# Kernel tuning notes

Hardware: AMD Instinct MI355X
Metric: run time of the kernel (lower is better)

## Reference

```python
import jax, jax.numpy as jnp
import numpy as np

ANCHOR = 12.0      # anchor (d,h,w) size used for parametrization
NMS_IOU = 0.25     # suppression threshold
TOPK = 2048        # pre-NMS candidate cap (= stop_after), fixed for jit


def setup_inputs() -> dict:
    key = jax.random.key(0)
    k1, k2 = jax.random.split(key)
    bboxes = jax.random.normal(k1, (2, 6, 64, 96, 96), dtype=jnp.float32)
    scores = jax.random.normal(k2, (2, 64, 96, 96), dtype=jnp.float32)
    return {"bboxes": bboxes, "scores": scores}


def _deparametrize(bboxes):
    # bboxes: (B, 6, D, H, W), parametrized as in Ren et al. 2017
    D, H, W = bboxes.shape[2:]
    axes = [jnp.arange(s, dtype=bboxes.dtype) + 0.5 for s in (D, H, W)]
    zyx = jnp.stack(jnp.meshgrid(*axes, indexing='ij'))        # (3, D, H, W)
    abs_zyx = bboxes[:, :3] * ANCHOR + zyx[None]               # center coords
    abs_dhw = jnp.exp(bboxes[:, 3:]) * ANCHOR                  # sizes
    return jnp.concatenate([abs_zyx, abs_dhw], axis=1)


def _pairwise_iou(b1, b2):
    # b1: (N,6), b2: (M,6) with (z,y,x,d,h,w)
    c1, s1 = b1[:, :3], b1[:, 3:]
    c2, s2 = b2[:, :3], b2[:, 3:]
    lo = jnp.maximum((c1 - s1 / 2)[:, None, :], (c2 - s2 / 2)[None, :, :])
    hi = jnp.minimum((c1 + s1 / 2)[:, None, :], (c2 + s2 / 2)[None, :, :])
    inter = jnp.clip(hi - lo, 0).prod(-1)                      # (N, M)
    union = s1.prod(-1)[:, None] + s2.prod(-1)[None, :] - inter
    return inter / union


def _nms_one(boxes_flat, scores_flat):
    # boxes_flat: (P, 6), scores_flat: (P,)
    scores_top, idx = jax.lax.top_k(scores_flat, TOPK)
    boxes_top = boxes_flat[idx]                                # (K, 6)
    ious = _pairwise_iou(boxes_top, boxes_top)                 # (K, K)
    ar = jnp.arange(TOPK)

    def body(keep, i):
        # suppress lower-scored boxes overlapping a kept box i
        suppress = (ious[i] > NMS_IOU) & (ar > i) & keep[i]
        return keep & ~suppress, None

    keep, _ = jax.lax.scan(body, jnp.ones(TOPK, dtype=bool), ar)
    out = jnp.concatenate([scores_top[:, None], boxes_top], axis=1)  # (K, 7)
    return jnp.where(keep[:, None], out, 0.0)


def reference(bboxes, scores):
    abs_boxes = _deparametrize(bboxes)                         # (B, 6, D, H, W)
    B = bboxes.shape[0]
    boxes_flat = abs_boxes.reshape(B, 6, -1).transpose(0, 2, 1)  # (B, P, 6)
    scores_flat = scores.reshape(B, -1)                          # (B, P)
    # (B, TOPK, 7): column 0 = score, columns 1:7 = (z,y,x,d,h,w); suppressed rows zeroed
    return jax.vmap(_nms_one)(boxes_flat, scores_flat)
```

## Files before the change

kernel.cpp:

```cpp
#include <hip/hip_runtime.h>
#include <math.h>

typedef unsigned int U32;
typedef unsigned long long U64;

constexpr int N_SP   = 64 * 96 * 96;
constexpr int NBATCH = 2;
constexpr int K_TOP  = 2048;
constexpr int NBINS  = 8192;
constexpr int CAP    = 8192;
constexpr float ANCHOR_F = 12.0f;
constexpr float NMS_IOU_F = 0.25f;

constexpr size_t OFF_HIST = 0;
constexpr size_t OFF_CNT  = OFF_HIST + 2 * NBINS * 4;
constexpr size_t OFF_THR  = OFF_CNT + 256;
constexpr size_t OFF_RANK = OFF_THR + 256;
constexpr size_t OFF_CAND = OFF_RANK + 2 * CAP * 4;
constexpr size_t OFF_BOX  = OFF_CAND + 2 * CAP * 8;
constexpr size_t OFF_MASK = OFF_BOX + 2 * 14 * K_TOP * 4;

__device__ __forceinline__ U32 mono_of(float f) {
  U32 u = __float_as_uint(f);
  return (u & 0x80000000u) ? ~u : (u | 0x80000000u);
}
__device__ __forceinline__ float un_mono(U32 m) {
  U32 u = (m & 0x80000000u) ? (m ^ 0x80000000u) : ~m;
  return __uint_as_float(u);
}

__global__ void __launch_bounds__(256) k_zero(U32* hist, U32* rank, U32* cnt) {
  int g = blockIdx.x * 256 + threadIdx.x;
  hist[g] = 0;
  rank[g] = 0;
  if (g < NBATCH) cnt[g] = 0;
}

__global__ void __launch_bounds__(256) k_hist(const float* __restrict__ scores,
                                              U32* __restrict__ hist) {
  int b = blockIdx.y;
  const float4* s4 = (const float4*)(scores + (size_t)b * N_SP)
                     + (size_t)blockIdx.x * 2048 + threadIdx.x;
  float4 v[8];
#pragma unroll
  for (int e = 0; e < 8; ++e) v[e] = s4[e * 256];
  __shared__ U32 lh[NBINS];
  for (int k = threadIdx.x; k < NBINS; k += 256) lh[k] = 0;
  __syncthreads();
#pragma unroll
  for (int e = 0; e < 8; ++e) {
    atomicAdd(&lh[mono_of(v[e].x) >> 19], 1u);
    atomicAdd(&lh[mono_of(v[e].y) >> 19], 1u);
    atomicAdd(&lh[mono_of(v[e].z) >> 19], 1u);
    atomicAdd(&lh[mono_of(v[e].w) >> 19], 1u);
  }
  __syncthreads();
  U32* gh = hist + (size_t)b * NBINS;
  for (int k = threadIdx.x; k < NBINS; k += 256) {
    U32 c = lh[k];
    if (c) atomicAdd(&gh[k], c);
  }
}

__global__ void __launch_bounds__(256) k_thresh(const U32* __restrict__ hist,
                                                U32* __restrict__ thr) {
  int b = blockIdx.x;
  const U32* h = hist + (size_t)b * NBINS;
  __shared__ U32 part[256];
  int t = threadIdx.x;
  int base = NBINS - 32 * (t + 1);
  U32 s = 0;
  for (int k = 0; k < 32; ++k) s += h[base + k];
  part[t] = s;
  __syncthreads();
  if (t == 0) {
    U32 cum = 0, bin = 0;
    for (int c = 0; c < 256; ++c) {
      U32 p = part[c];
      if (cum + p >= (U32)K_TOP) {
        int hb = NBINS - 32 * c - 1;
        for (int k = 0; k < 32; ++k) {
          cum += h[hb - k];
          if (cum >= (U32)K_TOP) { bin = (U32)(hb - k); break; }
        }
        break;
      }
      cum += p;
    }
    thr[b] = bin;
  }
}

__global__ void __launch_bounds__(256) k_collect(const float* __restrict__ scores,
                                                 const U32* __restrict__ thr,
                                                 U32* __restrict__ cnt,
                                                 U64* __restrict__ cand) {
  int b = blockIdx.y;
  U32 tb = thr[b];
  const float4* s4 = (const float4*)(scores + (size_t)b * N_SP)
                     + (size_t)blockIdx.x * 1024 + threadIdx.x;
  float4 v[4];
#pragma unroll
  for (int e = 0; e < 4; ++e) v[e] = s4[e * 256];
  __shared__ U64 lbuf[4096];
  __shared__ U32 lcnt, lbase;
  if (threadIdx.x == 0) lcnt = 0;
  __syncthreads();
#pragma unroll
  for (int e = 0; e < 4; ++e) {
    U32 i0 = (blockIdx.x * 1024 + e * 256 + threadIdx.x) * 4;
    float vv[4] = {v[e].x, v[e].y, v[e].z, v[e].w};
#pragma unroll
    for (int c = 0; c < 4; ++c) {
      U32 m = mono_of(vv[c]);
      if ((m >> 19) >= tb) {
        U32 p = atomicAdd(&lcnt, 1u);
        lbuf[p] = ((U64)m << 32) | (U32)(~(i0 + c));
      }
    }
  }
  __syncthreads();
  if (threadIdx.x == 0 && lcnt) lbase = atomicAdd(&cnt[b], lcnt);
  __syncthreads();
  U32 n = lcnt;
  if (n == 0) return;
  U32 base = lbase;
  U64* cb = cand + (size_t)b * CAP;
  for (U32 k = threadIdx.x; k < n; k += 256) {
    U32 pos = base + k;
    if (pos < (U32)CAP) cb[pos] = lbuf[k];
  }
}

__global__ void __launch_bounds__(256) k_count(const U64* __restrict__ cand,
                                               const U32* __restrict__ cnt,
                                               U32* __restrict__ rank) {
  int b = blockIdx.y;
  U32 C = cnt[b]; if (C > (U32)CAP) C = CAP;
  U32 g = blockIdx.x * 256 + threadIdx.x;
  U32 t = g & (CAP - 1);
  U32 sgm = g >> 13;
  if (t >= C) return;
  const U64* cb = cand + (size_t)b * CAP;
  U64 key = cb[t];
  U32 segLen = (C + 7) >> 3;
  U32 j0 = sgm * segLen;
  U32 j1 = j0 + segLen; if (j1 > C) j1 = C;
  U32 c = 0;
  for (U32 j = j0; j < j1; ++j) c += (cb[j] > key) ? 1u : 0u;
  if (c) atomicAdd(&rank[(size_t)b * CAP + t], c);
}

#pragma clang fp contract(off)

__global__ void __launch_bounds__(256) k_gather(const float* __restrict__ bboxes,
                                                const U64* __restrict__ cand,
                                                const U32* __restrict__ cnt,
                                                const U32* __restrict__ rank,
                                                float* __restrict__ box) {
  int b = blockIdx.y;
  U32 C = cnt[b]; if (C > (U32)CAP) C = CAP;
  U32 t = blockIdx.x * 256 + threadIdx.x;
  if (t >= C) return;
  U32 r = rank[(size_t)b * CAP + t];
  if (r >= (U32)K_TOP) return;
  U64 key = cand[(size_t)b * CAP + t];
  U32 idx = ~(U32)(key & 0xFFFFFFFFull);
  float sc = un_mono((U32)(key >> 32));
  int d = idx / 9216;
  int rem = idx - d * 9216;
  int h = rem / 96;
  int w = rem - h * 96;
  const float* src = bboxes + (size_t)b * 6 * N_SP + idx;
  float r0 = src[0];
  float r1 = src[(size_t)N_SP];
  float r2 = src[(size_t)2 * N_SP];
  float r3 = src[(size_t)3 * N_SP];
  float r4 = src[(size_t)4 * N_SP];
  float r5 = src[(size_t)5 * N_SP];
  float cz = r0 * ANCHOR_F + ((float)d + 0.5f);
  float cy = r1 * ANCHOR_F + ((float)h + 0.5f);
  float cx = r2 * ANCHOR_F + ((float)w + 0.5f);
  float sz = (float)exp((double)r3) * ANCHOR_F;
  float sy = (float)exp((double)r4) * ANCHOR_F;
  float sx = (float)exp((double)r5) * ANCHOR_F;
  float* B0 = box + (size_t)b * 14 * K_TOP;
  B0[0 * K_TOP + r] = cz;  B0[1 * K_TOP + r] = cy;  B0[2 * K_TOP + r] = cx;
  B0[3 * K_TOP + r] = sz;  B0[4 * K_TOP + r] = sy;  B0[5 * K_TOP + r] = sx;
  B0[6 * K_TOP + r] = cz - sz * 0.5f;
  B0[7 * K_TOP + r] = cy - sy * 0.5f;
  B0[8 * K_TOP + r] = cx - sx * 0.5f;
  B0[9 * K_TOP + r] = cz + sz * 0.5f;
  B0[10 * K_TOP + r] = cy + sy * 0.5f;
  B0[11 * K_TOP + r] = cx + sx * 0.5f;
  B0[12 * K_TOP + r] = (sz * sy) * sx;
  B0[13 * K_TOP + r] = sc;
}

__global__ void __launch_bounds__(256) k_mask(const float* __restrict__ box,
                                              U32* __restrict__ mask) {
  int b = blockIdx.y;
  int it = blockIdx.x >> 2;
  int jq = blockIdx.x & 3;
  const float* B0 = box + (size_t)b * 14 * K_TOP;
  __shared__ float ls[7][512];
  int j0 = jq * 512;
  for (int k = threadIdx.x; k < 7 * 512; k += 256) {
    int a = k >> 9, j = k & 511;
    ls[a][j] = B0[(size_t)(6 + a) * K_TOP + j0 + j];
  }
  __syncthreads();
  int lane = threadIdx.x & 63;
  int wv = threadIdx.x >> 6;
  int i = it * 64 + lane;
  float imin0 = B0[6 * K_TOP + i], imin1 = B0[7 * K_TOP + i], imin2 = B0[8 * K_TOP + i];
  float imax0 = B0[9 * K_TOP + i], imax1 = B0[10 * K_TOP + i], imax2 = B0[11 * K_TOP + i];
  float ivol  = B0[12 * K_TOP + i];
  U32 wbits[4];
  int jb = wv * 128;
#pragma unroll
  for (int wl = 0; wl < 4; ++wl) {
    U32 bits = 0;
    for (int bit = 0; bit < 32; ++bit) {
      int jl = jb + wl * 32 + bit;
      int j = j0 + jl;
      float lo0 = fmaxf(imin0, ls[0][jl]);
      float lo1 = fmaxf(imin1, ls[1][jl]);
      float lo2 = fmaxf(imin2, ls[2][jl]);
      float hi0 = fminf(imax0, ls[3][jl]);
      float hi1 = fminf(imax1, ls[4][jl]);
      float hi2 = fminf(imax2, ls[5][jl]);
      float d0 = fmaxf(hi0 - lo0, 0.0f);
      float d1 = fmaxf(hi1 - lo1, 0.0f);
      float d2 = fmaxf(hi2 - lo2, 0.0f);
      float inter = (d0 * d1) * d2;
      float uni = (ivol + ls[6][jl]) - inter;
      float iou = inter / uni;
      bits |= ((iou > NMS_IOU_F) && (j > i)) ? (1u << bit) : 0u;
    }
    wbits[wl] = bits;
  }
  uint4* mrow = (uint4*)(mask + ((size_t)(b * K_TOP + i)) * 64);
  mrow[jq * 4 + wv] = make_uint4(wbits[0], wbits[1], wbits[2], wbits[3]);
}

__global__ void __launch_bounds__(256) k_nms(const float* __restrict__ box,
                                             const U32* __restrict__ mask,
                                             float* __restrict__ out) {
  int b = blockIdx.x;
  int tid = threadIdx.x;
  const U32* mk = mask + (size_t)b * K_TOP * 64;
  __shared__ U32 buf[2][128 * 64];
  {
    const uint4* g = (const uint4*)mk;
    uint4* dst = (uint4*)buf[0];
    for (int k = tid; k < 2048; k += 256) dst[k] = g[k];
  }
  __syncthreads();
  U32 keep = 0xFFFFFFFFu;
  for (int c = 0; c < 16; ++c) {
    if (tid >= 64) {
      if (c + 1 < 16) {
        const uint4* g = (const uint4*)(mk + (size_t)(c + 1) * 8192);
        uint4* dst = (uint4*)buf[(c + 1) & 1];
        for (int k = tid - 64; k < 2048; k += 192) dst[k] = g[k];
      }
    } else {
      const U32* bs = buf[c & 1];
      for (int wb = 0; wb < 4; ++wb) {
        int w = c * 4 + wb;
        U32 kw = __shfl(keep, w);
#pragma unroll
        for (int bit = 0; bit < 32; ++bit) {
          U32 m = bs[(wb * 32 + bit) * 64 + tid];
          U32 mw = __shfl(m, w);
          U32 neg = (kw & (1u << bit)) ? 0xFFFFFFFFu : 0u;
          keep &= ~(m & neg);
          kw &= ~(mw & neg);
        }
      }
    }
    __syncthreads();
  }
  U32* keepArr = &buf[0][0];
  if (tid < 64) keepArr[tid] = keep;
  __syncthreads();
  const float* B0 = box + (size_t)b * 14 * K_TOP;
  for (int t = tid; t < K_TOP; t += 256) {
    U32 kp = (keepArr[t >> 5] >> (t & 31)) & 1u;
    float sc = B0[13 * K_TOP + t];
    float vz = B0[0 * K_TOP + t], vy = B0[1 * K_TOP + t], vx = B0[2 * K_TOP + t];
    float dz = B0[3 * K_TOP + t], dy = B0[4 * K_TOP + t], dx = B0[5 * K_TOP + t];
    float* o = out + (size_t)(b * K_TOP + t) * 7;
    o[0] = kp ? sc : 0.0f;
    o[1] = kp ? vz : 0.0f;
    o[2] = kp ? vy : 0.0f;
    o[3] = kp ? vx : 0.0f;
    o[4] = kp ? dz : 0.0f;
    o[5] = kp ? dy : 0.0f;
    o[6] = kp ? dx : 0.0f;
  }
}

extern "C" void kernel_launch(void* const* d_in, const int* in_sizes, int n_in,
                              void* d_out, int out_size, void* d_ws, size_t ws_size,
                              hipStream_t stream) {
  const float* bboxes = (const float*)d_in[0];
  const float* scores = (const float*)d_in[1];
  float* out = (float*)d_out;

  char* ws = (char*)d_ws;
  U32* hist = (U32*)(ws + OFF_HIST);
  U32* cnt  = (U32*)(ws + OFF_CNT);
  U32* thr  = (U32*)(ws + OFF_THR);
  U32* rank = (U32*)(ws + OFF_RANK);
  U64* cand = (U64*)(ws + OFF_CAND);
  float* box = (float*)(ws + OFF_BOX);
  U32* mask = (U32*)(ws + OFF_MASK);

  k_zero<<<64, 256, 0, stream>>>(hist, rank, cnt);
  k_hist<<<dim3(72, NBATCH), 256, 0, stream>>>(scores, hist);
  k_thresh<<<NBATCH, 256, 0, stream>>>(hist, thr);
  k_collect<<<dim3(144, NBATCH), 256, 0, stream>>>(scores, thr, cnt, cand);
  k_count<<<dim3(256, NBATCH), 256, 0, stream>>>(cand, cnt, rank);
  k_gather<<<dim3(CAP / 256, NBATCH), 256, 0, stream>>>(bboxes, cand, cnt, rank, box);
  k_mask<<<dim3(128, NBATCH), 256, 0, stream>>>(box, mask);
  k_nms<<<NBATCH, 256, 0, stream>>>(box, mask, out);
}
```

Before: 201.8 us.

## Transpose suppression mask and resolve NMS words with scalar readlane

The IoU mask is now written transposed (word-major, box-minor). The NMS kernel stages it into XOR-swizzled shared memory so each lane reads the 32 rows of its own word. Each 32-box word group is resolved on the diagonal word with scalar readlane operations, then applied to all lanes with one OR-reduction. This replaces the serial per-bit shuffle chain, shortening the dependent critical path at the cost of more registers and scattered global mask writes.

```diff
diff --git a/kernel.cpp b/kernel.cpp
--- a/kernel.cpp
+++ b/kernel.cpp
@@ -240,8 +240,12 @@
     }
     wbits[wl] = bits;
   }
-  uint4* mrow = (uint4*)(mask + ((size_t)(b * K_TOP + i)) * 64);
-  mrow[jq * 4 + wv] = make_uint4(wbits[0], wbits[1], wbits[2], wbits[3]);
+  U32* mT = mask + (size_t)b * 64 * K_TOP;
+#pragma unroll
+  for (int wl = 0; wl < 4; ++wl) {
+    int w = jq * 16 + wv * 4 + wl;
+    mT[(size_t)w * K_TOP + i] = wbits[wl];
+  }
 }
 
 __global__ void __launch_bounds__(256) k_nms(const float* __restrict__ box,
@@ -249,35 +253,66 @@
                                              float* __restrict__ out) {
   int b = blockIdx.x;
   int tid = threadIdx.x;
-  const U32* mk = mask + (size_t)b * K_TOP * 64;
-  __shared__ U32 buf[2][128 * 64];
-  {
-    const uint4* g = (const uint4*)mk;
-    uint4* dst = (uint4*)buf[0];
-    for (int k = tid; k < 2048; k += 256) dst[k] = g[k];
-  }
-  __syncthreads();
+  const U32* mkT = mask + (size_t)b * 64 * K_TOP;
+  __shared__ U32 buf[2][64 * 128];
+
+  for (int k = tid; k < 2048; k += 256) {
+    int w = k >> 5, seg = k & 31;
+    uint4 v = *(const uint4*)(mkT + (size_t)w * K_TOP + seg * 4);
+    U32* d = &buf[0][w * 128];
+    int r0 = seg * 4, sw = w & 31;
+    d[(r0 + 0) ^ sw] = v.x;
+    d[(r0 + 1) ^ sw] = v.y;
+    d[(r0 + 2) ^ sw] = v.z;
+    d[(r0 + 3) ^ sw] = v.w;
+  }
+  __syncthreads();
+
   U32 keep = 0xFFFFFFFFu;
   for (int c = 0; c < 16; ++c) {
     if (tid >= 64) {
       if (c + 1 < 16) {
-        const uint4* g = (const uint4*)(mk + (size_t)(c + 1) * 8192);
-        uint4* dst = (uint4*)buf[(c + 1) & 1];
-        for (int k = tid - 64; k < 2048; k += 192) dst[k] = g[k];
+        U32* dstbuf = buf[(c + 1) & 1];
+        for (int k = tid - 64; k < 2048; k += 192) {
+          int w = k >> 5, seg = k & 31;
+          uint4 v = *(const uint4*)(mkT + (size_t)w * K_TOP + (c + 1) * 128 + seg * 4);
+          U32* d = &dstbuf[w * 128];
+          int r0 = seg * 4, sw = w & 31;
+          d[(r0 + 0) ^ sw] = v.x;
+          d[(r0 + 1) ^ sw] = v.y;
+          d[(r0 + 2) ^ sw] = v.z;
+          d[(r0 + 3) ^ sw] = v.w;
+        }
       }
     } else {
-      const U32* bs = buf[c & 1];
-      for (int wb = 0; wb < 4; ++wb) {
-        int w = c * 4 + wb;
-        U32 kw = __shfl(keep, w);
-#pragma unroll
-        for (int bit = 0; bit < 32; ++bit) {
-          U32 m = bs[(wb * 32 + bit) * 64 + tid];
-          U32 mw = __shfl(m, w);
-          U32 neg = (kw & (1u << bit)) ? 0xFFFFFFFFu : 0u;
-          keep &= ~(m & neg);
-          kw &= ~(mw & neg);
+      const U32* row = &buf[c & 1][tid * 128];
+      U32 swz = (U32)(tid & 31);
+      U32 rw[32];
+#pragma unroll
+      for (int q = 0; q < 32; ++q) rw[q] = row[(U32)q ^ swz];
+#pragma unroll
+      for (int kk = 0; kk < 4; ++kk) {
+        U32 nx[32];
+        if (kk < 3) {
+#pragma unroll
+          for (int q = 0; q < 32; ++q) nx[q] = row[(U32)((kk + 1) * 32 + q) ^ swz];
         }
+        int g = c * 4 + kk;
+        U32 kw = (U32)__builtin_amdgcn_readlane((int)keep, g);
+        U32 dg[32];
+#pragma unroll
+        for (int q = 0; q < 32; ++q) dg[q] = (U32)__builtin_amdgcn_readlane((int)rw[q], g);
+#pragma unroll
+        for (int q = 0; q < 32; ++q) kw = (kw & (1u << q)) ? (kw & ~dg[q]) : kw;
+        U32 acc = 0;
+#pragma unroll
+        for (int q = 0; q < 32; ++q) {
+          U32 sel = (kw & (1u << q)) ? 0xFFFFFFFFu : 0u;
+          acc |= sel & rw[q];
+        }
+        keep &= ~acc;
+#pragma unroll
+        for (int q = 0; q < 32; ++q) if (kk < 3) rw[q] = nx[q];
       }
     }
     __syncthreads();
```

After: 214.6 us. 1.06x slower.

## Rewrite NMS sweep as single-wave register pipeline with readlane block resolution

Applied to the files above, without the earlier changes.

The greedy suppression sweep now runs in a single 64-lane wave. Mask rows are streamed directly from global memory into four rotating register buffers, replacing the LDS double buffer, the producer waves and the per-chunk block barriers. Within each 32-box diagonal block, the diagonal words are broadcast with readlane and resolved in a scalar-style serial loop, followed by one OR-reduction to apply suppression. This removes per-bit shuffles and the syncthreads calls, but it raises register pressure (128+ VGPRs) and relies on enough loads in flight to hide global latency.

```diff
diff --git a/kernel.cpp b/kernel.cpp
--- a/kernel.cpp
+++ b/kernel.cpp
@@ -250,41 +250,53 @@
   int b = blockIdx.x;
   int tid = threadIdx.x;
   const U32* mk = mask + (size_t)b * K_TOP * 64;
-  __shared__ U32 buf[2][128 * 64];
-  {
-    const uint4* g = (const uint4*)mk;
-    uint4* dst = (uint4*)buf[0];
-    for (int k = tid; k < 2048; k += 256) dst[k] = g[k];
-  }
-  __syncthreads();
-  U32 keep = 0xFFFFFFFFu;
-  for (int c = 0; c < 16; ++c) {
-    if (tid >= 64) {
-      if (c + 1 < 16) {
-        const uint4* g = (const uint4*)(mk + (size_t)(c + 1) * 8192);
-        uint4* dst = (uint4*)buf[(c + 1) & 1];
-        for (int k = tid - 64; k < 2048; k += 192) dst[k] = g[k];
-      }
-    } else {
-      const U32* bs = buf[c & 1];
-      for (int wb = 0; wb < 4; ++wb) {
-        int w = c * 4 + wb;
-        U32 kw = __shfl(keep, w);
-#pragma unroll
-        for (int bit = 0; bit < 32; ++bit) {
-          U32 m = bs[(wb * 32 + bit) * 64 + tid];
-          U32 mw = __shfl(m, w);
-          U32 neg = (kw & (1u << bit)) ? 0xFFFFFFFFu : 0u;
-          keep &= ~(m & neg);
-          kw &= ~(mw & neg);
-        }
-      }
+  __shared__ U32 keepArr[64];
+
+  if (tid < 64) {
+    int lane = tid;
+    U32 keep = 0xFFFFFFFFu;
+    U32 bufA[32], bufB[32], bufC[32], bufD[32];
+
+#define LOADB(R, blk)                                                          \
+  do {                                                                         \
+    if ((blk) < 64) {                                                          \
+      _Pragma("unroll") for (int q = 0; q < 32; ++q)                           \
+          R[q] = mk[((size_t)((blk) * 32 + q)) * 64 + lane];                   \
+    }                                                                          \
+  } while (0)
+
+#define COMPUTE(R, g)                                                          \
+  do {                                                                         \
+    U32 kw = (U32)__builtin_amdgcn_readlane((int)keep, (g));                   \
+    U32 dg[32];                                                                \
+    _Pragma("unroll") for (int q = 0; q < 32; ++q)                             \
+        dg[q] = (U32)__builtin_amdgcn_readlane((int)R[q], (g));                \
+    _Pragma("unroll") for (int q = 0; q < 32; ++q)                             \
+        kw = (kw & (1u << q)) ? (kw & ~dg[q]) : kw;                            \
+    U32 acc = 0;                                                               \
+    _Pragma("unroll") for (int q = 0; q < 32; ++q) {                           \
+      U32 sel = (kw & (1u << q)) ? 0xFFFFFFFFu : 0u;                           \
+      acc |= sel & R[q];                                                       \
+    }                                                                          \
+    keep &= ~acc;                                                              \
+  } while (0)
+
+    LOADB(bufA, 0);
+    LOADB(bufB, 1);
+    LOADB(bufC, 2);
+    LOADB(bufD, 3);
+    for (int g = 0; g < 64; g += 4) {
+      COMPUTE(bufA, g);     LOADB(bufA, g + 4);
+      COMPUTE(bufB, g + 1); LOADB(bufB, g + 5);
+      COMPUTE(bufC, g + 2); LOADB(bufC, g + 6);
+      COMPUTE(bufD, g + 3); LOADB(bufD, g + 7);
     }
-    __syncthreads();
-  }
-  U32* keepArr = &buf[0][0];
-  if (tid < 64) keepArr[tid] = keep;
-  __syncthreads();
+#undef LOADB
+#undef COMPUTE
+    keepArr[lane] = keep;
+  }
+  __syncthreads();
+
   const float* B0 = box + (size_t)b * 14 * K_TOP;
   for (int t = tid; t < K_TOP; t += 256) {
     U32 kp = (keepArr[t >> 5] >> (t & 31)) & 1u;
```

Measured after the change: 202.0 us. Within noise of the previous version (+0.1%).

## Use scalar readlane diagonal resolve and direct global-to-LDS loads in NMS scan

Applied to the files above, without the earlier changes.

The serial NMS scan used to do a per-bit shuffle chain for each 32-bit word. It now loads 32 mask rows into registers and resolves the diagonal word with scalar readlanes on a uniform keep word. It then ORs the kept rows into one accumulator, which cuts the serial dependency chain and removes the cross-lane shuffles. The mask staging also switches to the global_load_lds builtin, which writes 16-byte loads from global memory straight into LDS without going through VGPRs. The cost is higher register pressure from the two 32-element arrays.

```diff
diff --git a/kernel.cpp b/kernel.cpp
--- a/kernel.cpp
+++ b/kernel.cpp
@@ -249,42 +249,61 @@
                                              float* __restrict__ out) {
   int b = blockIdx.x;
   int tid = threadIdx.x;
+  int wv = tid >> 6, lane = tid & 63;
   const U32* mk = mask + (size_t)b * K_TOP * 64;
-  __shared__ U32 buf[2][128 * 64];
-  {
-    const uint4* g = (const uint4*)mk;
-    uint4* dst = (uint4*)buf[0];
-    for (int k = tid; k < 2048; k += 256) dst[k] = g[k];
-  }
-  __syncthreads();
+  __shared__ U32 sbuf[2][128 * 64];
+  __shared__ U32 keepArr[64];
+
+#define STAGE(cc, FIRST, STEP)                                                 \
+  do {                                                                         \
+    U32* dst = sbuf[(cc) & 1];                                                 \
+    const U32* gsrc = mk + (size_t)(cc) * 8192;                                \
+    for (int ins = (FIRST); ins < 32; ins += (STEP)) {                         \
+      __builtin_amdgcn_global_load_lds(                                        \
+          (const __attribute__((address_space(1))) U32*)(gsrc + ins * 256 +    \
+                                                         lane * 4),            \
+          (__attribute__((address_space(3))) U32*)(dst + ins * 256), 16, 0, 0);\
+    }                                                                          \
+  } while (0)
+
+  STAGE(0, wv, 4);
+  __syncthreads();
+
   U32 keep = 0xFFFFFFFFu;
   for (int c = 0; c < 16; ++c) {
-    if (tid >= 64) {
-      if (c + 1 < 16) {
-        const uint4* g = (const uint4*)(mk + (size_t)(c + 1) * 8192);
-        uint4* dst = (uint4*)buf[(c + 1) & 1];
-        for (int k = tid - 64; k < 2048; k += 192) dst[k] = g[k];
-      }
+    if (wv != 0) {
+      if (c + 1 < 16) STAGE(c + 1, wv - 1, 3);
     } else {
-      const U32* bs = buf[c & 1];
-      for (int wb = 0; wb < 4; ++wb) {
-        int w = c * 4 + wb;
-        U32 kw = __shfl(keep, w);
-#pragma unroll
-        for (int bit = 0; bit < 32; ++bit) {
-          U32 m = bs[(wb * 32 + bit) * 64 + tid];
-          U32 mw = __shfl(m, w);
-          U32 neg = (kw & (1u << bit)) ? 0xFFFFFFFFu : 0u;
-          keep &= ~(m & neg);
-          kw &= ~(mw & neg);
+      const U32* base = sbuf[c & 1];
+      for (int blk = 0; blk < 4; ++blk) {
+        int g = c * 4 + blk;
+        U32 rw[32];
+#pragma unroll
+        for (int q = 0; q < 32; ++q) rw[q] = base[(blk * 32 + q) * 64 + lane];
+        U32 kw = (U32)__builtin_amdgcn_readlane((int)keep, g);
+        U32 dg[32];
+#pragma unroll
+        for (int q = 0; q < 32; ++q)
+          dg[q] = (U32)__builtin_amdgcn_readlane((int)rw[q], g);
+#pragma unroll
+        for (int q = 0; q < 32; ++q)
+          kw = (kw & (1u << q)) ? (kw & ~dg[q]) : kw;
+        U32 acc = 0;
+#pragma unroll
+        for (int q = 0; q < 32; ++q) {
+          U32 sel = (kw & (1u << q)) ? 0xFFFFFFFFu : 0u;
+          acc |= sel & rw[q];
         }
+        keep &= ~acc;
       }
     }
     __syncthreads();
   }
-  U32* keepArr = &buf[0][0];
-  if (tid < 64) keepArr[tid] = keep;
-  __syncthreads();
+#undef STAGE
+
+  if (wv == 0) keepArr[lane] = keep;
+  __syncthreads();
+
   const float* B0 = box + (size_t)b * 14 * K_TOP;
   for (int t = tid; t < K_TOP; t += 256) {
     U32 kp = (keepArr[t >> 5] >> (t & 31)) & 1u;
```

New measurement: 204.4 us. About the same (+1.3%).
